# Optimization experiments

Measured on AMD Instinct MI355X. Metric: run time of the kernel, lower is better.

Reference implementation:

```python
import jax, jax.numpy as jnp
import numpy as np

N_CENTROIDS = 1024
NSAMPLES = 32
RADIUS = 0.5
BN_EPS = 1e-5


def fps(xyz, npoint):
    """Iterative farthest point sampling. xyz: [B,N,3] -> idx [B,npoint] int32."""
    B, N, _ = xyz.shape

    def step(carry, _):
        dist_min, farthest = carry  # [B,N], [B]
        centroid = jnp.take_along_axis(xyz, farthest[:, None, None], axis=1)  # [B,1,3]
        d = jnp.sum((xyz - centroid) ** 2, axis=-1)  # [B,N]
        dist_min = jnp.minimum(dist_min, d)
        nxt = jnp.argmax(dist_min, axis=1).astype(jnp.int32)
        return (dist_min, nxt), farthest

    init = (jnp.full((B, N), 1e10, xyz.dtype), jnp.zeros((B,), jnp.int32))
    _, idx = jax.lax.scan(step, init, None, length=npoint)
    return idx.T  # [B, npoint]


def gather_points(p, idx):
    """p: [B,N,C], idx: [B,...] int -> [B,...,C]."""
    return jax.vmap(lambda pp, ii: pp[ii])(p, idx)


def square_distance(a, b):
    """a: [B,S,3], b: [B,N,3] -> [B,S,N] squared distances (GEMM form)."""
    aa = jnp.sum(a * a, axis=-1)[:, :, None]
    bb = jnp.sum(b * b, axis=-1)[:, None, :]
    ab = jnp.einsum('bsc,bnc->bsn', a, b)
    return aa + bb - 2.0 * ab


def ball_query(centroids, xyz, nsample, radius):
    B, S, _ = centroids.shape
    N = xyz.shape[1]
    sqrdists = square_distance(centroids, xyz)  # [B,S,N]
    base = jnp.broadcast_to(jnp.arange(N, dtype=jnp.int32), (B, S, N))
    group_idx = jnp.where(sqrdists > radius * radius, N, base)
    group_idx = jnp.sort(group_idx, axis=-1)[:, :, :nsample]  # [B,S,K]
    first = group_idx[:, :, :1]
    group_idx = jnp.where(group_idx == N, first, group_idx)
    return group_idx


def batchnorm2d(h, gamma, beta):
    """Training-mode BN over (B,H,W) per channel. h: [B,C,H,W]."""
    mean = jnp.mean(h, axis=(0, 2, 3), keepdims=True)
    var = jnp.mean((h - mean) ** 2, axis=(0, 2, 3), keepdims=True)
    hhat = (h - mean) * jax.lax.rsqrt(var + BN_EPS)
    return gamma[None, :, None, None] * hhat + beta[None, :, None, None]


def conv1x1(h, w, b):
    """h: [B,C,H,W], w: [O,C] -> [B,O,H,W]."""
    return jnp.einsum('bchw,oc->bohw', h, w) + b[None, :, None, None]


def setup_inputs() -> dict:
    key = jax.random.key(0)
    ks = jax.random.split(key, 4)
    B, N, D = 16, 4096, 3
    mlp0, mlp1, in_ch = 64, 128, 6
    return {
        'x': jax.random.normal(ks[0], (B, N, 3), jnp.float32),
        'points': jax.random.normal(ks[1], (B, N, D), jnp.float32),
        'w1': jax.random.normal(ks[2], (mlp0, in_ch), jnp.float32) * 0.1,
        'b1': jnp.zeros((mlp0,), jnp.float32),
        'gamma1': jnp.ones((mlp0,), jnp.float32),
        'beta1': jnp.zeros((mlp0,), jnp.float32),
        'w2': jax.random.normal(ks[3], (mlp1, mlp0), jnp.float32) * 0.1,
        'b2': jnp.zeros((mlp1,), jnp.float32),
        'gamma2': jnp.ones((mlp1,), jnp.float32),
        'beta2': jnp.zeros((mlp1,), jnp.float32),
    }


def reference(x, points, w1, b1, gamma1, beta1, w2, b2, gamma2, beta2):
    # FPS -> centroids
    cidx = fps(x, N_CENTROIDS)                      # [B,S]
    centroids = gather_points(x, cidx)              # [B,S,3]
    # Ball-query grouping
    idx = ball_query(centroids, x, NSAMPLES, RADIUS)  # [B,S,K]
    grouped_xyz = gather_points(x, idx) - centroids[:, :, None, :]  # [B,S,K,3]
    grouped_pts = jnp.concatenate([grouped_xyz, gather_points(points, idx)], axis=-1)  # [B,S,K,C]
    # g_points.transpose(1,3): [B,S,K,C] -> [B,C,K,S]
    h = jnp.transpose(grouped_pts, (0, 3, 2, 1))
    h = jax.nn.relu(batchnorm2d(conv1x1(h, w1, b1), gamma1, beta1))
    h = jax.nn.relu(batchnorm2d(conv1x1(h, w2, b2), gamma2, beta2))
    out = jnp.max(h, axis=2)            # [B,mlp1,S]
    out = jnp.transpose(out, (0, 2, 1))  # [B,S,mlp1]
    return centroids, out
```

## Files before the change

### kernel.cpp

```cpp
#include <hip/hip_runtime.h>
#include <stdint.h>
#include <math.h>

constexpr int BB = 16;
constexpr int NN = 4096;
constexpr int SS = 1024;
constexpr int KK = 32;
constexpr int C3 = 128;
constexpr float R2 = 0.25f;
constexpr int STAT_BLOCKS = 2048;

typedef float v2f __attribute__((ext_vector_type(2)));

__device__ __forceinline__ float sumsq3(float x, float y, float z) {
#pragma clang fp contract(off)
  return (x * x + y * y) + z * z;
}

__device__ __forceinline__ v2f sumsq3p(v2f x, v2f y, v2f z) {
#pragma clang fp contract(off)
  return (x * x + y * y) + z * z;
}

__device__ __forceinline__ float ball_d(float aa, float bb, float cx, float cy,
                                        float cz, float px, float py, float pz) {
#pragma clang fp contract(off)
  float ab = (cx * px + cy * py) + cz * pz;
  return (aa + bb) - 2.0f * ab;
}

__device__ __forceinline__ unsigned long long u64max(unsigned long long a,
                                                     unsigned long long b) {
  return a > b ? a : b;
}

#define DPP_KEY_STEP(CTRL, k)                                                  \
  {                                                                            \
    int lo_ = (int)(unsigned)(k);                                              \
    int hi_ = (int)(unsigned)((k) >> 32);                                      \
    int slo_ = __builtin_amdgcn_update_dpp(0, lo_, (CTRL), 0xf, 0xf, true);    \
    int shi_ = __builtin_amdgcn_update_dpp(0, hi_, (CTRL), 0xf, 0xf, true);    \
    unsigned long long o_ =                                                    \
        ((unsigned long long)(unsigned)shi_ << 32) | (unsigned)(unsigned)slo_; \
    (k) = u64max((k), o_);                                                     \
  }

__device__ __forceinline__ unsigned long long readlane_key(unsigned lo,
                                                           unsigned hi,
                                                           int lane) {
  unsigned l = (unsigned)__builtin_amdgcn_readlane((int)lo, lane);
  unsigned h = (unsigned)__builtin_amdgcn_readlane((int)hi, lane);
  return ((unsigned long long)h << 32) | l;
}

__global__ __launch_bounds__(256) void k_fps(const float* __restrict__ x,
                                             float* __restrict__ outc,
                                             float* __restrict__ aa) {
  __shared__ float4 xs4[NN];
  __shared__ unsigned long long wkey[2][4];
  __shared__ int farhist[SS];
  int b = blockIdx.x, t = threadIdx.x;
  const float* xb = x + (size_t)b * NN * 3;
  v2f px2[8], py2[8], pz2[8], dm2[8];
#pragma unroll
  for (int i = 0; i < 8; ++i) {
    int n0 = t + (2 * i) * 256, n1 = t + (2 * i + 1) * 256;
    float a0 = xb[3 * n0], a1 = xb[3 * n0 + 1], a2 = xb[3 * n0 + 2];
    float b0 = xb[3 * n1], b1 = xb[3 * n1 + 1], b2 = xb[3 * n1 + 2];
    px2[i] = (v2f){a0, b0}; py2[i] = (v2f){a1, b1}; pz2[i] = (v2f){a2, b2};
    dm2[i] = (v2f){1e10f, 1e10f};
    xs4[n0] = make_float4(a0, a1, a2, 0.f);
    xs4[n1] = make_float4(b0, b1, b2, 0.f);
  }
  if (t == 0) farhist[0] = 0;
  __syncthreads();
  int far = 0;
  int w = t >> 6;
  unsigned base = (unsigned)(NN - 1 - t);
  for (int it = 1; it < SS; ++it) {
    float4 c4 = xs4[far];
    v2f cx2 = (v2f){c4.x, c4.x}, cy2 = (v2f){c4.y, c4.y}, cz2 = (v2f){c4.z, c4.z};
    float best = -1.0f;
    int bj = 0;
#pragma unroll
    for (int i = 0; i < 8; ++i) {
      v2f dx = px2[i] - cx2, dy = py2[i] - cy2, dz = pz2[i] - cz2;
      v2f d = sumsq3p(dx, dy, dz);
      v2f dm = dm2[i];
      dm.x = fminf(dm.x, d.x);
      dm.y = fminf(dm.y, d.y);
      dm2[i] = dm;
      if (dm.x > best) { best = dm.x; bj = 2 * i; }
      if (dm.y > best) { best = dm.y; bj = 2 * i + 1; }
    }
    unsigned blo = base - ((unsigned)bj << 8);
    unsigned long long key =
        ((unsigned long long)__float_as_uint(best) << 32) | blo;
    DPP_KEY_STEP(0xB1, key);
    DPP_KEY_STEP(0x4E, key);
    DPP_KEY_STEP(0x124, key);
    DPP_KEY_STEP(0x128, key);
    {
      unsigned klo = (unsigned)key, khi = (unsigned)(key >> 32);
      unsigned long long r0 = readlane_key(klo, khi, 0);
      unsigned long long r1 = readlane_key(klo, khi, 16);
      unsigned long long r2 = readlane_key(klo, khi, 32);
      unsigned long long r3 = readlane_key(klo, khi, 48);
      key = u64max(u64max(r0, r1), u64max(r2, r3));
    }
    int buf = it & 1;
    if ((t & 63) == 0) wkey[buf][w] = key;
    __syncthreads();
    unsigned long long k0 = wkey[buf][0], k1 = wkey[buf][1];
    unsigned long long k2 = wkey[buf][2], k3 = wkey[buf][3];
    unsigned long long kk = u64max(u64max(k0, k1), u64max(k2, k3));
    far = NN - 1 - (int)(unsigned)(kk & 0xffffffffu);
    if (t == 0) farhist[it] = far;
  }
  __syncthreads();
  for (int i = t; i < SS; i += 256) {
    int n = farhist[i];
    float4 c4 = xs4[n];
    int gi = b * SS + i;
    outc[3 * gi] = c4.x; outc[3 * gi + 1] = c4.y; outc[3 * gi + 2] = c4.z;
    aa[gi] = sumsq3(c4.x, c4.y, c4.z);
  }
}

__global__ __launch_bounds__(256) void k_ball(const float* __restrict__ x,
                                              const float* __restrict__ cent,
                                              const float* __restrict__ aa,
                                              int* __restrict__ idx) {
  int gw = (blockIdx.x * 256 + threadIdx.x) >> 6;
  int lane = threadIdx.x & 63;
  if (gw >= BB * SS) return;
  int b = gw >> 10;
  const float* xb = x + (size_t)b * NN * 3;
  float cx = cent[3 * gw], cy = cent[3 * gw + 1], cz = cent[3 * gw + 2];
  float a = aa[gw];
  int* out = idx + (size_t)gw * KK;
  int found = 0, firstN = 0;
  for (int c0 = 0; c0 < NN && found < KK; c0 += 64) {
    int n = c0 + lane;
    float px = xb[3 * n], py = xb[3 * n + 1], pz = xb[3 * n + 2];
    float pb = sumsq3(px, py, pz);
    float d = ball_d(a, pb, cx, cy, cz, px, py, pz);
    bool pred = (d <= R2);
    unsigned long long m = __ballot(pred);
    if (found == 0 && m) firstN = c0 + (__ffsll((unsigned long long)m) - 1);
    if (pred) {
      int pos = found + __popcll(m & ((1ull << lane) - 1ull));
      if (pos < KK) out[pos] = n;
    }
    found += __popcll(m);
  }
  if (lane == 0 && found < KK) {
    for (int k = found; k < KK; ++k) out[k] = firstN;
  }
}

__global__ __launch_bounds__(256) void k_stats1(
    const float* __restrict__ x, const float* __restrict__ pts,
    const float* __restrict__ cent, const int* __restrict__ idx,
    const float* __restrict__ w1, const float* __restrict__ b1,
    float* __restrict__ partial1) {
  __shared__ float feat[KK][6];
  __shared__ float red[4][64][2];
  int t = threadIdx.x;
  int c = t & 63, kq = t >> 6;
  float w[6];
#pragma unroll
  for (int j = 0; j < 6; ++j) w[j] = w1[c * 6 + j];
  float bias = b1[c];
  float sum = 0.f, sq = 0.f;
  for (int gi = 0; gi < 8; ++gi) {
    int g = blockIdx.x * 8 + gi;
    int b = g >> 10;
    if (t < KK) {
      int n = idx[(size_t)g * KK + t];
      const float* p = x + ((size_t)b * NN + n) * 3;
      feat[t][0] = p[0] - cent[3 * g];
      feat[t][1] = p[1] - cent[3 * g + 1];
      feat[t][2] = p[2] - cent[3 * g + 2];
      const float* q = pts + ((size_t)b * NN + n) * 3;
      feat[t][3] = q[0];
      feat[t][4] = q[1];
      feat[t][5] = q[2];
    }
    __syncthreads();
    for (int k = kq * 8; k < kq * 8 + 8; ++k) {
      float a = bias;
#pragma unroll
      for (int j = 0; j < 6; ++j) a += w[j] * feat[k][j];
      sum += a;
      sq += a * a;
    }
    __syncthreads();
  }
  red[kq][c][0] = sum;
  red[kq][c][1] = sq;
  __syncthreads();
  if (t < 64) {
    float s = ((red[0][t][0] + red[1][t][0]) + red[2][t][0]) + red[3][t][0];
    float q = ((red[0][t][1] + red[1][t][1]) + red[2][t][1]) + red[3][t][1];
    partial1[(size_t)(blockIdx.x * 64 + t) * 2] = s;
    partial1[(size_t)(blockIdx.x * 64 + t) * 2 + 1] = q;
  }
}

__global__ void k_red1(const float* __restrict__ partial1,
                       const float* __restrict__ gamma, const float* __restrict__ beta,
                       float* __restrict__ sc1) {
  __shared__ double rd[64][4][2];
  int t = threadIdx.x;
  int c = t & 63, q = t >> 6;
  double s = 0.0, qq = 0.0;
  for (int blk = q * 512; blk < q * 512 + 512; ++blk) {
    s += partial1[(size_t)(blk * 64 + c) * 2];
    qq += partial1[(size_t)(blk * 64 + c) * 2 + 1];
  }
  rd[c][q][0] = s; rd[c][q][1] = qq;
  __syncthreads();
  if (t < 64) {
    double S = ((rd[t][0][0] + rd[t][1][0]) + rd[t][2][0]) + rd[t][3][0];
    double Q = ((rd[t][0][1] + rd[t][1][1]) + rd[t][2][1]) + rd[t][3][1];
    const double cnt = (double)BB * KK * SS;
    double mean = S / cnt;
    double var = Q / cnt - mean * mean;
    float scale = gamma[t] * (float)(1.0 / sqrt(var + 1e-5));
    float shift = beta[t] - (float)mean * scale;
    sc1[t] = scale;
    sc1[64 + t] = shift;
  }
}

__global__ __launch_bounds__(256) void k_stats2(
    const float* __restrict__ x, const float* __restrict__ pts,
    const float* __restrict__ cent, const int* __restrict__ idx,
    const float* __restrict__ w1, const float* __restrict__ b1,
    const float* __restrict__ sc1, const float* __restrict__ w2,
    const float* __restrict__ b2, float* __restrict__ partial2,
    float* __restrict__ gmax, float* __restrict__ gmin) {
  __shared__ float feat[KK][6];
  __shared__ float vT[64][36];
  __shared__ float w2sA[64][68];
  __shared__ float w2sB[64][68];
  __shared__ float red[C3][4][2];
  __shared__ float mx[C3][4], mn[C3][4];
  int t = threadIdx.x;
  int c1 = t & 63, kq = t >> 6;
  int c2p = t >> 2, ks = t & 3;
  {
    int r = t >> 1, h = (t & 1) * 32;
    float* dst = (r < 64 ? &w2sA[r][h] : &w2sB[r - 64][h]);
    const float* src = w2 + r * 64 + h;
    for (int c = 0; c < 32; ++c) dst[c] = src[c];
  }
  float w1r[6];
#pragma unroll
  for (int j = 0; j < 6; ++j) w1r[j] = w1[c1 * 6 + j];
  float bias1 = b1[c1];
  float scale1 = sc1[c1], shift1 = sc1[64 + c1];
  float bias2a = b2[c2p], bias2b = b2[c2p + 64];
  float sumA = 0.f, sqA = 0.f, sumB = 0.f, sqB = 0.f;
  for (int gi = 0; gi < 8; ++gi) {
    int g = blockIdx.x * 8 + gi;
    int b = g >> 10;
    if (t < KK) {
      int n = idx[(size_t)g * KK + t];
      const float* p = x + ((size_t)b * NN + n) * 3;
      feat[t][0] = p[0] - cent[3 * g];
      feat[t][1] = p[1] - cent[3 * g + 1];
      feat[t][2] = p[2] - cent[3 * g + 2];
      const float* q = pts + ((size_t)b * NN + n) * 3;
      feat[t][3] = q[0];
      feat[t][4] = q[1];
      feat[t][5] = q[2];
    }
    __syncthreads();
    for (int k = kq * 8; k < kq * 8 + 8; ++k) {
      float a = bias1;
#pragma unroll
      for (int j = 0; j < 6; ++j) a += w1r[j] * feat[k][j];
      vT[c1][k] = fmaxf(0.f, a * scale1 + shift1);
    }
    __syncthreads();
    float accA[8] = {0, 0, 0, 0, 0, 0, 0, 0};
    float accB[8] = {0, 0, 0, 0, 0, 0, 0, 0};
#pragma unroll
    for (int c0 = 0; c0 < 64; c0 += 4) {
      float4 wa4 = *(const float4*)&w2sA[c2p][c0];
      float4 wb4 = *(const float4*)&w2sB[c2p][c0];
#pragma unroll
      for (int cc = 0; cc < 4; ++cc) {
        int c = c0 + cc;
        float4 v0 = *(const float4*)&vT[c][ks * 8];
        float4 v1 = *(const float4*)&vT[c][ks * 8 + 4];
        float wa = (cc == 0 ? wa4.x : cc == 1 ? wa4.y : cc == 2 ? wa4.z : wa4.w);
        float wb = (cc == 0 ? wb4.x : cc == 1 ? wb4.y : cc == 2 ? wb4.z : wb4.w);
        accA[0] += wa * v0.x; accA[1] += wa * v0.y; accA[2] += wa * v0.z; accA[3] += wa * v0.w;
        accA[4] += wa * v1.x; accA[5] += wa * v1.y; accA[6] += wa * v1.z; accA[7] += wa * v1.w;
        accB[0] += wb * v0.x; accB[1] += wb * v0.y; accB[2] += wb * v0.z; accB[3] += wb * v0.w;
        accB[4] += wb * v1.x; accB[5] += wb * v1.y; accB[6] += wb * v1.z; accB[7] += wb * v1.w;
      }
    }
    float mA = -1e30f, mB = -1e30f, nA = 1e30f, nB = 1e30f;
#pragma unroll
    for (int i = 0; i < 8; ++i) {
      float a = accA[i] + bias2a;
      sumA += a; sqA += a * a;
      mA = fmaxf(mA, a); nA = fminf(nA, a);
      float c_ = accB[i] + bias2b;
      sumB += c_; sqB += c_ * c_;
      mB = fmaxf(mB, c_); nB = fminf(nB, c_);
    }
    mx[c2p][ks] = mA;      mn[c2p][ks] = nA;
    mx[c2p + 64][ks] = mB; mn[c2p + 64][ks] = nB;
    __syncthreads();
    if (t < C3) {
      float M = fmaxf(fmaxf(mx[t][0], mx[t][1]), fmaxf(mx[t][2], mx[t][3]));
      float m_ = fminf(fminf(mn[t][0], mn[t][1]), fminf(mn[t][2], mn[t][3]));
      gmax[(size_t)g * C3 + t] = M;
      gmin[(size_t)g * C3 + t] = m_;
    }
  }
  red[c2p][ks][0] = sumA;      red[c2p][ks][1] = sqA;
  red[c2p + 64][ks][0] = sumB; red[c2p + 64][ks][1] = sqB;
  __syncthreads();
  if (t < C3) {
    float s = ((red[t][0][0] + red[t][1][0]) + red[t][2][0]) + red[t][3][0];
    float q = ((red[t][0][1] + red[t][1][1]) + red[t][2][1]) + red[t][3][1];
    partial2[(size_t)(blockIdx.x * 128 + t) * 2] = s;
    partial2[(size_t)(blockIdx.x * 128 + t) * 2 + 1] = q;
  }
}

__global__ void k_red2(const float* __restrict__ partial2,
                       const float* __restrict__ gamma, const float* __restrict__ beta,
                       float* __restrict__ sc2) {
  __shared__ double rd[128][4][2];
  int t = threadIdx.x;
  int c = t & 127, q = t >> 7;
  double s = 0.0, qq = 0.0;
  for (int blk = q * 512; blk < q * 512 + 512; ++blk) {
    s += partial2[(size_t)(blk * 128 + c) * 2];
    qq += partial2[(size_t)(blk * 128 + c) * 2 + 1];
  }
  rd[c][q][0] = s; rd[c][q][1] = qq;
  __syncthreads();
  if (t < 128) {
    double S = ((rd[t][0][0] + rd[t][1][0]) + rd[t][2][0]) + rd[t][3][0];
    double Q = ((rd[t][0][1] + rd[t][1][1]) + rd[t][2][1]) + rd[t][3][1];
    const double cnt = (double)BB * KK * SS;
    double mean = S / cnt;
    double var = Q / cnt - mean * mean;
    float scale = gamma[t] * (float)(1.0 / sqrt(var + 1e-5));
    float shift = beta[t] - (float)mean * scale;
    sc2[t] = scale;
    sc2[128 + t] = shift;
  }
}

__global__ void k_final2(const float* __restrict__ gmin,
                         const float* __restrict__ sc2, float* __restrict__ outp) {
  int i = blockIdx.x * blockDim.x + threadIdx.x;
  if (i >= BB * SS * C3) return;
  int c = i & (C3 - 1);
  float scale = sc2[c], shift = sc2[C3 + c];
  float a = (scale >= 0.f) ? outp[i] : gmin[i];
  outp[i] = fmaxf(0.f, a * scale + shift);
}

extern "C" void kernel_launch(void* const* d_in, const int* in_sizes, int n_in,
                              void* d_out, int out_size, void* d_ws, size_t ws_size,
                              hipStream_t stream) {
  const float* x      = (const float*)d_in[0];
  const float* pts    = (const float*)d_in[1];
  const float* w1     = (const float*)d_in[2];
  const float* b1     = (const float*)d_in[3];
  const float* gamma1 = (const float*)d_in[4];
  const float* beta1  = (const float*)d_in[5];
  const float* w2     = (const float*)d_in[6];
  const float* b2     = (const float*)d_in[7];
  const float* gamma2 = (const float*)d_in[8];
  const float* beta2  = (const float*)d_in[9];

  float* out_cent = (float*)d_out;
  float* out_feat = (float*)d_out + (size_t)BB * SS * 3;

  char* w = (char*)d_ws;
  float* aa    = (float*)w; w += (size_t)BB * SS * 4;
  int* idx     = (int*)w;   w += (size_t)BB * SS * KK * 4;
  float* p1    = (float*)w; w += (size_t)STAT_BLOCKS * 64 * 2 * 4;
  float* p2    = (float*)w; w += (size_t)STAT_BLOCKS * 128 * 2 * 4;
  float* sc1   = (float*)w; w += 64 * 2 * 4;
  float* sc2   = (float*)w; w += 128 * 2 * 4;
  float* gmin  = (float*)w; w += (size_t)BB * SS * C3 * 4;

  k_fps<<<BB, 256, 0, stream>>>(x, out_cent, aa);
  k_ball<<<(BB * SS) / 4, 256, 0, stream>>>(x, out_cent, aa, idx);
  k_stats1<<<STAT_BLOCKS, 256, 0, stream>>>(x, pts, out_cent, idx, w1, b1, p1);
  k_red1<<<1, 256, 0, stream>>>(p1, gamma1, beta1, sc1);
  k_stats2<<<STAT_BLOCKS, 256, 0, stream>>>(x, pts, out_cent, idx, w1, b1, sc1,
                                            w2, b2, p2, out_feat, gmin);
  k_red2<<<1, 512, 0, stream>>>(p2, gamma2, beta2, sc2);
  k_final2<<<(BB * SS * C3 + 255) / 256, 256, 0, stream>>>(gmin, sc2, out_feat);
}
```

Measured before the change: 902.6 us.

## Fuse ball query into BN1 stats kernel and widen final reductions

Merges the ball-query kernel into the first BN statistics kernel: each block of 8 groups runs the ball query per wave, keeps the neighbor indices in shared memory, and then computes the conv1 stats from them without re-reading idx from global memory. This removes one launch and one global round-trip for the indices. It also widens the single-block BN reductions k_red1 and k_red2 to 1024 threads so each thread sums fewer partials serially. The fused kernel does the ball query with fewer waves in flight per centroid, and the double-precision sum order changes slightly.

```diff
diff --git a/kernel.cpp b/kernel.cpp
--- a/kernel.cpp
+++ b/kernel.cpp
@@ -127,57 +127,55 @@
   }
 }
 
-__global__ __launch_bounds__(256) void k_ball(const float* __restrict__ x,
-                                              const float* __restrict__ cent,
-                                              const float* __restrict__ aa,
-                                              int* __restrict__ idx) {
-  int gw = (blockIdx.x * 256 + threadIdx.x) >> 6;
-  int lane = threadIdx.x & 63;
-  if (gw >= BB * SS) return;
-  int b = gw >> 10;
-  const float* xb = x + (size_t)b * NN * 3;
-  float cx = cent[3 * gw], cy = cent[3 * gw + 1], cz = cent[3 * gw + 2];
-  float a = aa[gw];
-  int* out = idx + (size_t)gw * KK;
-  int found = 0, firstN = 0;
-  for (int c0 = 0; c0 < NN && found < KK; c0 += 64) {
-    int n = c0 + lane;
-    float px = xb[3 * n], py = xb[3 * n + 1], pz = xb[3 * n + 2];
-    float pb = sumsq3(px, py, pz);
-    float d = ball_d(a, pb, cx, cy, cz, px, py, pz);
-    bool pred = (d <= R2);
-    unsigned long long m = __ballot(pred);
-    if (found == 0 && m) firstN = c0 + (__ffsll((unsigned long long)m) - 1);
-    if (pred) {
-      int pos = found + __popcll(m & ((1ull << lane) - 1ull));
-      if (pos < KK) out[pos] = n;
-    }
-    found += __popcll(m);
-  }
-  if (lane == 0 && found < KK) {
-    for (int k = found; k < KK; ++k) out[k] = firstN;
-  }
-}
-
-__global__ __launch_bounds__(256) void k_stats1(
+__global__ __launch_bounds__(256) void k_ballstats1(
     const float* __restrict__ x, const float* __restrict__ pts,
-    const float* __restrict__ cent, const int* __restrict__ idx,
+    const float* __restrict__ cent, const float* __restrict__ aa,
     const float* __restrict__ w1, const float* __restrict__ b1,
-    float* __restrict__ partial1) {
+    int* __restrict__ idx, float* __restrict__ partial1) {
+  __shared__ int sidx[8][KK];
   __shared__ float feat[KK][6];
   __shared__ float red[4][64][2];
   int t = threadIdx.x;
+  int w = t >> 6, lane = t & 63;
+  for (int qq = 0; qq < 2; ++qq) {
+    int q = w + qq * 4;
+    int g = blockIdx.x * 8 + q;
+    int b = g >> 10;
+    const float* xb = x + (size_t)b * NN * 3;
+    float cx = cent[3 * g], cy = cent[3 * g + 1], cz = cent[3 * g + 2];
+    float a = aa[g];
+    int* gout = idx + (size_t)g * KK;
+    int found = 0, firstN = 0;
+    for (int c0 = 0; c0 < NN && found < KK; c0 += 64) {
+      int n = c0 + lane;
+      float px = xb[3 * n], py = xb[3 * n + 1], pz = xb[3 * n + 2];
+      float pb = sumsq3(px, py, pz);
+      float d = ball_d(a, pb, cx, cy, cz, px, py, pz);
+      bool pred = (d <= R2);
+      unsigned long long m = __ballot(pred);
+      if (found == 0 && m) firstN = c0 + (__ffsll((unsigned long long)m) - 1);
+      if (pred) {
+        int pos = found + __popcll(m & ((1ull << lane) - 1ull));
+        if (pos < KK) { gout[pos] = n; sidx[q][pos] = n; }
+      }
+      found += __popcll(m);
+    }
+    if (lane == 0 && found < KK) {
+      for (int k = found; k < KK; ++k) { gout[k] = firstN; sidx[q][k] = firstN; }
+    }
+  }
+  __syncthreads();
   int c = t & 63, kq = t >> 6;
-  float w[6];
-#pragma unroll
-  for (int j = 0; j < 6; ++j) w[j] = w1[c * 6 + j];
+  float wv[6];
+#pragma unroll
+  for (int j = 0; j < 6; ++j) wv[j] = w1[c * 6 + j];
   float bias = b1[c];
   float sum = 0.f, sq = 0.f;
   for (int gi = 0; gi < 8; ++gi) {
     int g = blockIdx.x * 8 + gi;
     int b = g >> 10;
     if (t < KK) {
-      int n = idx[(size_t)g * KK + t];
+      int n = sidx[gi][t];
       const float* p = x + ((size_t)b * NN + n) * 3;
       feat[t][0] = p[0] - cent[3 * g];
       feat[t][1] = p[1] - cent[3 * g + 1];
@@ -191,7 +189,7 @@
     for (int k = kq * 8; k < kq * 8 + 8; ++k) {
       float a = bias;
 #pragma unroll
-      for (int j = 0; j < 6; ++j) a += w[j] * feat[k][j];
+      for (int j = 0; j < 6; ++j) a += wv[j] * feat[k][j];
       sum += a;
       sq += a * a;
     }
@@ -211,19 +209,20 @@
 __global__ void k_red1(const float* __restrict__ partial1,
                        const float* __restrict__ gamma, const float* __restrict__ beta,
                        float* __restrict__ sc1) {
-  __shared__ double rd[64][4][2];
+  __shared__ double rd[64][16][2];
   int t = threadIdx.x;
   int c = t & 63, q = t >> 6;
   double s = 0.0, qq = 0.0;
-  for (int blk = q * 512; blk < q * 512 + 512; ++blk) {
+  for (int blk = q * 128; blk < q * 128 + 128; ++blk) {
     s += partial1[(size_t)(blk * 64 + c) * 2];
     qq += partial1[(size_t)(blk * 64 + c) * 2 + 1];
   }
   rd[c][q][0] = s; rd[c][q][1] = qq;
   __syncthreads();
   if (t < 64) {
-    double S = ((rd[t][0][0] + rd[t][1][0]) + rd[t][2][0]) + rd[t][3][0];
-    double Q = ((rd[t][0][1] + rd[t][1][1]) + rd[t][2][1]) + rd[t][3][1];
+    double S = 0.0, Q = 0.0;
+#pragma unroll
+    for (int i = 0; i < 16; ++i) { S += rd[t][i][0]; Q += rd[t][i][1]; }
     const double cnt = (double)BB * KK * SS;
     double mean = S / cnt;
     double var = Q / cnt - mean * mean;
@@ -338,19 +337,20 @@
 __global__ void k_red2(const float* __restrict__ partial2,
                        const float* __restrict__ gamma, const float* __restrict__ beta,
                        float* __restrict__ sc2) {
-  __shared__ double rd[128][4][2];
+  __shared__ double rd[128][8][2];
   int t = threadIdx.x;
   int c = t & 127, q = t >> 7;
   double s = 0.0, qq = 0.0;
-  for (int blk = q * 512; blk < q * 512 + 512; ++blk) {
+  for (int blk = q * 256; blk < q * 256 + 256; ++blk) {
     s += partial2[(size_t)(blk * 128 + c) * 2];
     qq += partial2[(size_t)(blk * 128 + c) * 2 + 1];
   }
   rd[c][q][0] = s; rd[c][q][1] = qq;
   __syncthreads();
   if (t < 128) {
-    double S = ((rd[t][0][0] + rd[t][1][0]) + rd[t][2][0]) + rd[t][3][0];
-    double Q = ((rd[t][0][1] + rd[t][1][1]) + rd[t][2][1]) + rd[t][3][1];
+    double S = 0.0, Q = 0.0;
+#pragma unroll
+    for (int i = 0; i < 8; ++i) { S += rd[t][i][0]; Q += rd[t][i][1]; }
     const double cnt = (double)BB * KK * SS;
     double mean = S / cnt;
     double var = Q / cnt - mean * mean;
@@ -398,11 +398,11 @@
   float* gmin  = (float*)w; w += (size_t)BB * SS * C3 * 4;
 
   k_fps<<<BB, 256, 0, stream>>>(x, out_cent, aa);
-  k_ball<<<(BB * SS) / 4, 256, 0, stream>>>(x, out_cent, aa, idx);
-  k_stats1<<<STAT_BLOCKS, 256, 0, stream>>>(x, pts, out_cent, idx, w1, b1, p1);
-  k_red1<<<1, 256, 0, stream>>>(p1, gamma1, beta1, sc1);
+  k_ballstats1<<<STAT_BLOCKS, 256, 0, stream>>>(x, pts, out_cent, aa, w1, b1,
+                                                idx, p1);
+  k_red1<<<1, 1024, 0, stream>>>(p1, gamma1, beta1, sc1);
   k_stats2<<<STAT_BLOCKS, 256, 0, stream>>>(x, pts, out_cent, idx, w1, b1, sc1,
                                             w2, b2, p2, out_feat, gmin);
-  k_red2<<<1, 512, 0, stream>>>(p2, gamma2, beta2, sc2);
+  k_red2<<<1, 1024, 0, stream>>>(p2, gamma2, beta2, sc2);
   k_final2<<<(BB * SS * C3 + 255) / 256, 256, 0, stream>>>(gmin, sc2, out_feat);
 }
```

After: 894.2 us (median of 2 runs). No clear change (-0.9%).
